# Performance work log

Hardware: AMD Instinct MI355X
Metric: run time of the kernel (lower is better)

## Reference

```python
import jax, jax.numpy as jnp
import numpy as np

VOCAB = 67
EMB = 32
BRANCH = 32
OUT = 96
L = 16
B = 131072


def setup_inputs() -> dict:
    key = jax.random.key(0)
    ks = jax.random.split(key, 10)
    x = jax.random.randint(ks[0], (B, L), 0, VOCAB, dtype=jnp.int64)
    embed = jax.random.normal(ks[1], (VOCAB, EMB), dtype=jnp.float32) * 0.1
    w2 = jax.random.normal(ks[2], (BRANCH, EMB, 2), dtype=jnp.float32) * 0.1
    b2 = jnp.zeros((BRANCH,), jnp.float32)
    w3 = jax.random.normal(ks[3], (BRANCH, EMB, 3), dtype=jnp.float32) * 0.1
    b3 = jnp.zeros((BRANCH,), jnp.float32)
    w4 = jax.random.normal(ks[4], (BRANCH, EMB, 4), dtype=jnp.float32) * 0.1
    b4 = jnp.zeros((BRANCH,), jnp.float32)
    pw = jax.random.normal(ks[5], (OUT, 3 * BRANCH), dtype=jnp.float32) * 0.02
    pb = jnp.zeros((OUT,), jnp.float32)
    return {"x": x, "embed": embed, "w2": w2, "b2": b2, "w3": w3,
            "b3": b3, "w4": w4, "b4": b4, "pw": pw, "pb": pb}


def _branch(emb_ncl, w, b):
    # emb_ncl: [B, EMB, L]; w: [BRANCH, EMB, k] -> conv valid, ReLU, max over time
    y = jax.lax.conv_general_dilated(
        emb_ncl, w, window_strides=(1,), padding='VALID',
        dimension_numbers=('NCH', 'OIH', 'NCH'))
    y = jax.nn.relu(y + b[None, :, None])
    return jnp.max(y, axis=2)  # [B, BRANCH]


def reference(x, embed, w2, b2, w3, b3, w4, b4, pw, pb):
    # padding_idx=0: row 0 of the table is zeros
    table = embed.at[0].set(0.0)
    emb = table[x]                      # [B, L, EMB]
    emb = jnp.transpose(emb, (0, 2, 1))  # [B, EMB, L]
    g2 = _branch(emb, w2, b2)
    g3 = _branch(emb, w3, b3)
    g4 = _branch(emb, w4, b4)
    feat = jnp.concatenate([g2, g3, g4], axis=1)  # [B, 96]
    # Linear + ReLU (dropout is identity at eval)
    return jax.nn.relu(feat @ pw.T + pb)
```

## Files before the change

### kernel.cpp

```cpp
#include <hip/hip_runtime.h>
#include <hip/hip_fp16.h>


#define VOCABSZ 67
#define EMBSZ   32
#define NCH     32
#define NFEAT   96
#define SEQL    16
#define BATCH   131072
#define NTAB    9
#define NENT    (NTAB * VOCABSZ)
#define TABU    (NENT * NCH / 2)
#define PWOFF   TABU
#define NFP     (NFEAT / 2)
#define NPW     (NFEAT * NFP)
#define LDSB    (NENT * 128)
#define TSTRB   (VOCABSZ * 128)

typedef _Float16 v2h __attribute__((ext_vector_type(2)));
typedef _Float16 v8h __attribute__((ext_vector_type(8)));
typedef float    v4f __attribute__((ext_vector_type(4)));

__device__ __forceinline__ unsigned packh2(float a, float b) {
    v2h p; p[0] = (_Float16)a; p[1] = (_Float16)b;
    return __builtin_bit_cast(unsigned, p);
}

__global__ __launch_bounds__(256) void build_tables(
    const float* __restrict__ embed,
    const float* __restrict__ w2, const float* __restrict__ b2,
    const float* __restrict__ w3, const float* __restrict__ b3,
    const float* __restrict__ w4, const float* __restrict__ b4,
    const float* __restrict__ pw,
    unsigned* __restrict__ ws)
{
    int idx = blockIdx.x * 256 + threadIdx.x;
    if (idx < TABU) {
        int cp = idx & 15;
        int t  = idx >> 4;
        int j  = t / VOCABSZ;
        int v  = t - j * VOCABSZ;
        const float* w; const float* bias; int k, h;
        if (j < 2)      { w = w2; k = 2; h = j;     bias = (h == 0) ? b2 : nullptr; }
        else if (j < 5) { w = w3; k = 3; h = j - 2; bias = (h == 0) ? b3 : nullptr; }
        else            { w = w4; k = 4; h = j - 5; bias = (h == 0) ? b4 : nullptr; }
        int c0 = 2 * cp;
        float a0 = bias ? bias[c0]     : 0.0f;
        float a1 = bias ? bias[c0 + 1] : 0.0f;
        if (v != 0) {
            #pragma unroll
            for (int e = 0; e < EMBSZ; ++e) {
                float ev = embed[v * EMBSZ + e];
                a0 += ev * w[((c0    ) * EMBSZ + e) * k + h];
                a1 += ev * w[((c0 + 1) * EMBSZ + e) * k + h];
            }
        }
        ws[t * 16 + cp] = packh2(a0, a1);
    } else if (idx < TABU + NPW) {
        int i  = idx - TABU;
        int o  = i / NFP;
        int fp = i - o * NFP;
        ws[PWOFF + i] = packh2(pw[o * NFEAT + 2 * fp], pw[o * NFEAT + 2 * fp + 1]);
    }
}

template<int K, int N, int P0, int TB>
__device__ __forceinline__ void convbatch(const char* __restrict__ base,
                                          const int (&ap)[16], v8h& m)
{
    v8h s[N];
    #pragma unroll
    for (int u = 0; u < N; ++u)
        s[u] = *reinterpret_cast<const v8h*>(base + TB + ap[P0 + u]);
    #pragma unroll
    for (int h = 1; h < K; ++h) {
        v8h t[N];
        #pragma unroll
        for (int u = 0; u < N; ++u)
            t[u] = *reinterpret_cast<const v8h*>(base + TB + h * TSTRB + ap[P0 + u + h]);
        #pragma unroll
        for (int u = 0; u < N; ++u) s[u] = s[u] + t[u];
    }
    #pragma unroll
    for (int u = 0; u < N; ++u) m = __builtin_elementwise_max(m, s[u]);
}

__global__ __launch_bounds__(512, 4) void fused_cnn(
    const int*      __restrict__ x,
    const unsigned* __restrict__ ws,
    const float*    __restrict__ pb,
    float*          __restrict__ out)
{
    extern __shared__ __align__(16) char ldsraw[];
    const int tid = threadIdx.x;
    {
        const float4* s4 = reinterpret_cast<const float4*>(ws);
        float4* d4 = reinterpret_cast<float4*>(ldsraw);
        #pragma unroll
        for (int i0 = 0; i0 < 2560; i0 += 512) {
            int i = i0 + tid;
            if (i < 2412) {
                int t = i >> 2;
                int c = (i + t) & 3;
                float4 v = s4[t * 4 + c];
                d4[t * 8 + c]     = v;
                d4[t * 8 + 4 + c] = v;
            }
        }
    }
    __syncthreads();

    const int lane = tid & 63;
    const int wv   = tid >> 6;
    const int ml   = lane & 15;
    const int c    = lane >> 4;
    const int par  = (lane >> 3) & 1;
    const int co   = (c << 4) + (par << 6);
    const int rowb = blockIdx.x * 128 + wv * 16;
    const int row  = rowb + ml;
    const char* base = ldsraw;

    const int4* xp = reinterpret_cast<const int4*>(x + row * SEQL);
    int4 q0 = xp[0], q1 = xp[1], q2 = xp[2], q3 = xp[3];
    int ap[16];
    ap[ 0] = (q0.x << 7) + co; ap[ 1] = (q0.y << 7) + co;
    ap[ 2] = (q0.z << 7) + co; ap[ 3] = (q0.w << 7) + co;
    ap[ 4] = (q1.x << 7) + co; ap[ 5] = (q1.y << 7) + co;
    ap[ 6] = (q1.z << 7) + co; ap[ 7] = (q1.w << 7) + co;
    ap[ 8] = (q2.x << 7) + co; ap[ 9] = (q2.y << 7) + co;
    ap[10] = (q2.z << 7) + co; ap[11] = (q2.w << 7) + co;
    ap[12] = (q3.x << 7) + co; ap[13] = (q3.y << 7) + co;
    ap[14] = (q3.z << 7) + co; ap[15] = (q3.w << 7) + co;

    v8h m2 = {}, m3 = {}, m4 = {};

    convbatch<2, 5,  0, 0 * TSTRB>(base, ap, m2);
    convbatch<2, 5,  5, 0 * TSTRB>(base, ap, m2);
    convbatch<2, 5, 10, 0 * TSTRB>(base, ap, m2);
    convbatch<3, 5,  0, 2 * TSTRB>(base, ap, m3);
    convbatch<3, 5,  5, 2 * TSTRB>(base, ap, m3);
    convbatch<3, 4, 10, 2 * TSTRB>(base, ap, m3);
    convbatch<4, 5,  0, 5 * TSTRB>(base, ap, m4);
    convbatch<4, 4,  5, 5 * TSTRB>(base, ap, m4);
    convbatch<4, 4,  9, 5 * TSTRB>(base, ap, m4);

    const unsigned* __restrict__ pwp = ws + PWOFF + ml * NFP + c * 4;
    #pragma unroll
    for (int u = 0; u < 6; ++u) {
        v4f acc = {0.f, 0.f, 0.f, 0.f};
        v8h b0 = *reinterpret_cast<const v8h*>(pwp + 768 * u);
        v8h b1 = *reinterpret_cast<const v8h*>(pwp + 768 * u + 16);
        v8h b2 = *reinterpret_cast<const v8h*>(pwp + 768 * u + 32);
        acc = __builtin_amdgcn_mfma_f32_16x16x32_f16(m2, b0, acc, 0, 0, 0);
        acc = __builtin_amdgcn_mfma_f32_16x16x32_f16(m3, b1, acc, 0, 0, 0);
        acc = __builtin_amdgcn_mfma_f32_16x16x32_f16(m4, b2, acc, 0, 0, 0);
        float pbl = pb[16 * u + ml];
        #pragma unroll
        for (int r = 0; r < 4; ++r)
            out[(size_t)(rowb + c * 4 + r) * NFEAT + 16 * u + ml] =
                fmaxf(acc[r] + pbl, 0.f);
    }
}

extern "C" void kernel_launch(void* const* d_in, const int* in_sizes, int n_in,
                              void* d_out, int out_size, void* d_ws, size_t ws_size,
                              hipStream_t stream)
{
    const int*   x     = (const int*)  d_in[0];
    const float* embed = (const float*)d_in[1];
    const float* w2    = (const float*)d_in[2];
    const float* b2    = (const float*)d_in[3];
    const float* w3    = (const float*)d_in[4];
    const float* b3    = (const float*)d_in[5];
    const float* w4    = (const float*)d_in[6];
    const float* b4    = (const float*)d_in[7];
    const float* pw    = (const float*)d_in[8];
    const float* pb    = (const float*)d_in[9];
    float* out = (float*)d_out;
    unsigned* ws = (unsigned*)d_ws;

    build_tables<<<(TABU + NPW + 255) / 256, 256, 0, stream>>>(
        embed, w2, b2, w3, b3, w4, b4, pw, ws);

    (void)hipFuncSetAttribute((const void*)fused_cnn,
                              hipFuncAttributeMaxDynamicSharedMemorySize,
                              LDSB);
    fused_cnn<<<BATCH / 128, 512, LDSB, stream>>>(x, ws, pb, out);
}
```

Baseline: 45.55 us.

## Split conv tables between LDS and global memory to shrink LDS and raise occupancy

Only the k=2 and k=3 tap tables (5 of 9) are now staged in LDS with a simpler duplicated layout, and the k=4 tables are read directly from the global workspace through the cache. This shrinks LDS per block from about 77 KB to about 43 KB, and launch bounds rise to 6 blocks per CU so more waves stay resident. The global and LDS gathers are interleaved to overlap their latencies. The trade is extra global/L2 gather traffic and the loss of the old bank-conflict-avoiding rotation for the k=4 branch.

New measurement: 63.50 us. 39.4% more time.

```diff
diff --git a/kernel.cpp b/kernel.cpp
--- a/kernel.cpp
+++ b/kernel.cpp
@@ -14,8 +14,10 @@
 #define PWOFF   TABU
 #define NFP     (NFEAT / 2)
 #define NPW     (NFEAT * NFP)
-#define LDSB    (NENT * 128)
-#define TSTRB   (VOCABSZ * 128)
+#define GTS     4288
+#define LTS     8576
+#define LDSB    (5 * LTS)
+#define G4BASE  (5 * GTS)
 
 typedef _Float16 v2h __attribute__((ext_vector_type(2)));
 typedef _Float16 v8h __attribute__((ext_vector_type(8)));
@@ -65,19 +67,19 @@
 }
 
 template<int K, int N, int P0, int TB>
-__device__ __forceinline__ void convbatch(const char* __restrict__ base,
-                                          const int (&ap)[16], v8h& m)
+__device__ __forceinline__ void lconv(const char* __restrict__ base,
+                                      const int (&ag)[16], int kadj, v8h& m)
 {
     v8h s[N];
     #pragma unroll
     for (int u = 0; u < N; ++u)
-        s[u] = *reinterpret_cast<const v8h*>(base + TB + ap[P0 + u]);
+        s[u] = *reinterpret_cast<const v8h*>(base + TB + ((ag[P0 + u] << 1) + kadj));
     #pragma unroll
     for (int h = 1; h < K; ++h) {
         v8h t[N];
         #pragma unroll
         for (int u = 0; u < N; ++u)
-            t[u] = *reinterpret_cast<const v8h*>(base + TB + h * TSTRB + ap[P0 + u + h]);
+            t[u] = *reinterpret_cast<const v8h*>(base + TB + h * LTS + ((ag[P0 + u + h] << 1) + kadj));
         #pragma unroll
         for (int u = 0; u < N; ++u) s[u] = s[u] + t[u];
     }
@@ -85,7 +87,28 @@
     for (int u = 0; u < N; ++u) m = __builtin_elementwise_max(m, s[u]);
 }
 
-__global__ __launch_bounds__(512, 4) void fused_cnn(
+template<int K, int N, int P0>
+__device__ __forceinline__ void gconv(const char* __restrict__ g4,
+                                      const int (&ag)[16], v8h& m)
+{
+    v8h s[N];
+    #pragma unroll
+    for (int u = 0; u < N; ++u)
+        s[u] = *reinterpret_cast<const v8h*>(g4 + ag[P0 + u]);
+    #pragma unroll
+    for (int h = 1; h < K; ++h) {
+        v8h t[N];
+        #pragma unroll
+        for (int u = 0; u < N; ++u)
+            t[u] = *reinterpret_cast<const v8h*>(g4 + h * GTS + ag[P0 + u + h]);
+        #pragma unroll
+        for (int u = 0; u < N; ++u) s[u] = s[u] + t[u];
+    }
+    #pragma unroll
+    for (int u = 0; u < N; ++u) m = __builtin_elementwise_max(m, s[u]);
+}
+
+__global__ __launch_bounds__(512, 6) void fused_cnn(
     const int*      __restrict__ x,
     const unsigned* __restrict__ ws,
     const float*    __restrict__ pb,
@@ -97,12 +120,11 @@
         const float4* s4 = reinterpret_cast<const float4*>(ws);
         float4* d4 = reinterpret_cast<float4*>(ldsraw);
         #pragma unroll
-        for (int i0 = 0; i0 < 2560; i0 += 512) {
+        for (int i0 = 0; i0 < 1536; i0 += 512) {
             int i = i0 + tid;
-            if (i < 2412) {
-                int t = i >> 2;
-                int c = (i + t) & 3;
-                float4 v = s4[t * 4 + c];
+            if (i < 1340) {
+                int t = i >> 2, c = i & 3;
+                float4 v = s4[i];
                 d4[t * 8 + c]     = v;
                 d4[t * 8 + 4 + c] = v;
             }
@@ -115,34 +137,40 @@
     const int ml   = lane & 15;
     const int c    = lane >> 4;
     const int par  = (lane >> 3) & 1;
-    const int co   = (c << 4) + (par << 6);
+    const int kadj = (par << 6) - (c << 4);
+    const int co   = c << 4;
     const int rowb = blockIdx.x * 128 + wv * 16;
     const int row  = rowb + ml;
     const char* base = ldsraw;
+    const char* g4   = reinterpret_cast<const char*>(ws) + G4BASE;
 
     const int4* xp = reinterpret_cast<const int4*>(x + row * SEQL);
     int4 q0 = xp[0], q1 = xp[1], q2 = xp[2], q3 = xp[3];
-    int ap[16];
-    ap[ 0] = (q0.x << 7) + co; ap[ 1] = (q0.y << 7) + co;
-    ap[ 2] = (q0.z << 7) + co; ap[ 3] = (q0.w << 7) + co;
-    ap[ 4] = (q1.x << 7) + co; ap[ 5] = (q1.y << 7) + co;
-    ap[ 6] = (q1.z << 7) + co; ap[ 7] = (q1.w << 7) + co;
-    ap[ 8] = (q2.x << 7) + co; ap[ 9] = (q2.y << 7) + co;
-    ap[10] = (q2.z << 7) + co; ap[11] = (q2.w << 7) + co;
-    ap[12] = (q3.x << 7) + co; ap[13] = (q3.y << 7) + co;
-    ap[14] = (q3.z << 7) + co; ap[15] = (q3.w << 7) + co;
+    int ag[16];
+    ag[ 0] = (q0.x << 6) + co; ag[ 1] = (q0.y << 6) + co;
+    ag[ 2] = (q0.z << 6) + co; ag[ 3] = (q0.w << 6) + co;
+    ag[ 4] = (q1.x << 6) + co; ag[ 5] = (q1.y << 6) + co;
+    ag[ 6] = (q1.z << 6) + co; ag[ 7] = (q1.w << 6) + co;
+    ag[ 8] = (q2.x << 6) + co; ag[ 9] = (q2.y << 6) + co;
+    ag[10] = (q2.z << 6) + co; ag[11] = (q2.w << 6) + co;
+    ag[12] = (q3.x << 6) + co; ag[13] = (q3.y << 6) + co;
+    ag[14] = (q3.z << 6) + co; ag[15] = (q3.w << 6) + co;
 
     v8h m2 = {}, m3 = {}, m4 = {};
 
-    convbatch<2, 5,  0, 0 * TSTRB>(base, ap, m2);
-    convbatch<2, 5,  5, 0 * TSTRB>(base, ap, m2);
-    convbatch<2, 5, 10, 0 * TSTRB>(base, ap, m2);
-    convbatch<3, 5,  0, 2 * TSTRB>(base, ap, m3);
-    convbatch<3, 5,  5, 2 * TSTRB>(base, ap, m3);
-    convbatch<3, 4, 10, 2 * TSTRB>(base, ap, m3);
-    convbatch<4, 5,  0, 5 * TSTRB>(base, ap, m4);
-    convbatch<4, 4,  5, 5 * TSTRB>(base, ap, m4);
-    convbatch<4, 4,  9, 5 * TSTRB>(base, ap, m4);
+    gconv<4, 3,  0>(g4, ag, m4);
+    lconv<2, 4,  0, 0 * LTS>(base, ag, kadj, m2);
+    gconv<4, 3,  3>(g4, ag, m4);
+    lconv<2, 4,  4, 0 * LTS>(base, ag, kadj, m2);
+    gconv<4, 3,  6>(g4, ag, m4);
+    lconv<2, 4,  8, 0 * LTS>(base, ag, kadj, m2);
+    gconv<4, 2,  9>(g4, ag, m4);
+    lconv<2, 3, 12, 0 * LTS>(base, ag, kadj, m2);
+    gconv<4, 2, 11>(g4, ag, m4);
+    lconv<3, 4,  0, 2 * LTS>(base, ag, kadj, m3);
+    lconv<3, 4,  4, 2 * LTS>(base, ag, kadj, m3);
+    lconv<3, 3,  8, 2 * LTS>(base, ag, kadj, m3);
+    lconv<3, 3, 11, 2 * LTS>(base, ag, kadj, m3);
 
     const unsigned* __restrict__ pwp = ws + PWOFF + ml * NFP + c * 4;
     #pragma unroll
@@ -182,8 +210,5 @@
     build_tables<<<(TABU + NPW + 255) / 256, 256, 0, stream>>>(
         embed, w2, b2, w3, b3, w4, b4, pw, ws);
 
-    (void)hipFuncSetAttribute((const void*)fused_cnn,
-                              hipFuncAttributeMaxDynamicSharedMemorySize,
-                              LDSB);
     fused_cnn<<<BATCH / 128, 512, LDSB, stream>>>(x, ws, pb, out);
 }
```
